# Kernel optimization log

Hardware: AMD Instinct MI355X
Metric: run time of the kernel (lower is better)

Reference implementation:

```python
import jax, jax.numpy as jnp
import numpy as np
import math

B, T, C = 4, 2048, 1024
H = 16
HD = C // H


def setup_inputs() -> dict:
    key = jax.random.key(0)
    k1, k2, k3 = jax.random.split(key, 3)
    sc = 0.02
    return {
        "x": jax.random.normal(k1, (B, T, C), dtype=jnp.float32),
        "w_qkv": jax.random.normal(k2, (3 * C, C), dtype=jnp.float32) * sc,
        "b_qkv": jnp.zeros((3 * C,), dtype=jnp.float32),
        "w_proj": jax.random.normal(k3, (C, C), dtype=jnp.float32) * sc,
        "b_proj": jnp.zeros((C,), dtype=jnp.float32),
    }


def reference(x, w_qkv, b_qkv, w_proj, b_proj):
    b, t, c = x.shape
    qkv = x @ w_qkv.T + b_qkv            # [B,T,3C]
    q, k, v = jnp.split(qkv, 3, axis=2)
    # [B,T,C] -> [B,H,T,HD]
    def heads(z):
        return z.reshape(b, t, H, HD).transpose(0, 2, 1, 3)
    q, k, v = heads(q), heads(k), heads(v)
    att = jnp.einsum('bhqd,bhkd->bhqk', q, k) / math.sqrt(HD)
    causal = jnp.tril(jnp.ones((t, t), dtype=bool))
    att = jnp.where(causal[None, None], att, -jnp.inf)
    att = jax.nn.softmax(att, axis=-1)   # dropout p=0 (eval)
    y = jnp.einsum('bhqk,bhkd->bhqd', att, v)
    y = y.transpose(0, 2, 1, 3).reshape(b, t, c)
    return y @ w_proj.T + b_proj
```

## Files before the change

### kernel.cpp

```cpp
#include <hip/hip_runtime.h>
#include <hip/hip_bf16.h>

#define B_ 4
#define T_ 2048
#define C_ 1024
#define H_ 16
#define HD_ 64
#define M_ (B_*T_)

typedef __attribute__((ext_vector_type(8))) short short8;
typedef __attribute__((ext_vector_type(4))) float f32x4;
typedef __attribute__((ext_vector_type(16))) float f32x16;
typedef __attribute__((ext_vector_type(4))) unsigned int u32x4;
typedef unsigned short u16;
typedef unsigned int u32;

__device__ __forceinline__ u16 f2bf(float f){
  unsigned int x = __builtin_bit_cast(unsigned int, f);
  x += 0x7fffu + ((x >> 16) & 1u);
  return (u16)(x >> 16);
}

__device__ __forceinline__ u32 cvtpk(float lo, float hi){
  u32 r;
  asm("v_cvt_pk_bf16_f32 %0, %1, %2" : "=v"(r) : "v"(lo), "v"(hi));
  return r;
}

#define GLOAD_LDS(gsrc, ldst) \
  __builtin_amdgcn_global_load_lds((const __attribute__((address_space(1))) u32*)(gsrc), \
                                   (__attribute__((address_space(3))) u32*)(ldst), 16, 0, 0)

__global__ __launch_bounds__(256)
void cvt3_kernel(const float* __restrict__ x, const float* __restrict__ w1,
                 const float* __restrict__ w2, u16* __restrict__ xb,
                 u16* __restrict__ w1b, u16* __restrict__ w2b){
  int i = blockIdx.x * 256 + threadIdx.x;
  const float* src; u16* dst; int off;
  if (i < 2097152)              { src = x;  dst = xb;  off = i; }
  else if (i < 2097152 + 786432){ src = w1; dst = w1b; off = i - 2097152; }
  else                          { src = w2; dst = w2b; off = i - (2097152 + 786432); }
  float4 f = reinterpret_cast<const float4*>(src)[off];
  ushort4 u;
  u.x = f2bf(f.x); u.y = f2bf(f.y); u.z = f2bf(f.z); u.w = f2bf(f.w);
  reinterpret_cast<ushort4*>(dst)[off] = u;
}

template<int MODE>
__global__ __launch_bounds__(256)
void gemm_bt(const u16* __restrict__ A, const u16* __restrict__ Bt,
             const float* __restrict__ bias, float* __restrict__ Cf,
             u16* __restrict__ Qo, u16* __restrict__ Ko, u16* __restrict__ Vo,
             int N, int K)
{
  __shared__ u16 As[128 * 64];
  __shared__ u16 Bs[128 * 64];
  const int tid = threadIdx.x;
  const int wave = tid >> 6, lane = tid & 63;
  const int lo = lane & 15, hi = lane >> 4;
  const int wm = (wave >> 1) * 64, wn = (wave & 1) * 64;

  const int nwgx = gridDim.x;
  const int nwg  = gridDim.x * gridDim.y;
  const int flat = blockIdx.y * nwgx + blockIdx.x;
  const int cpx  = nwg >> 3;
  const int swz  = (flat & 7) * cpx + (flat >> 3);
  const long bm = (long)(swz / nwgx) * 128, bn = (long)(swz % nwgx) * 128;

  f32x4 acc[4][4];
  #pragma unroll
  for (int i = 0; i < 4; i++)
    #pragma unroll
    for (int j = 0; j < 4; j++)
      acc[i][j] = (f32x4){0.f, 0.f, 0.f, 0.f};

  for (int k0 = 0; k0 < K; k0 += 64){
    if (k0) __syncthreads();
    #pragma unroll
    for (int j = 0; j < 4; j++){
      int chunk = j * 256 + tid;
      int row = chunk >> 3, cc = (chunk & 7) * 8;
      GLOAD_LDS(&A [(bm + row) * K + k0 + cc], &As[chunk * 8]);
      GLOAD_LDS(&Bt[(bn + row) * K + k0 + cc], &Bs[chunk * 8]);
    }
    __syncthreads();
    #pragma unroll
    for (int kk = 0; kk < 64; kk += 32){
      short8 af[4], bf[4];
      #pragma unroll
      for (int mi = 0; mi < 4; mi++)
        af[mi] = *reinterpret_cast<const short8*>(&As[(wm + mi*16 + lo) * 64 + kk + hi*8]);
      #pragma unroll
      for (int ni = 0; ni < 4; ni++)
        bf[ni] = *reinterpret_cast<const short8*>(&Bs[(wn + ni*16 + lo) * 64 + kk + hi*8]);
      #pragma unroll
      for (int mi = 0; mi < 4; mi++)
        #pragma unroll
        for (int ni = 0; ni < 4; ni++)
          acc[mi][ni] = __builtin_amdgcn_mfma_f32_16x16x32_bf16(af[mi], bf[ni], acc[mi][ni], 0, 0, 0);
    }
  }

  #pragma unroll
  for (int mi = 0; mi < 4; mi++){
    #pragma unroll
    for (int ni = 0; ni < 4; ni++){
      #pragma unroll
      for (int rg = 0; rg < 4; rg++){
        long rowg = bm + wm + mi*16 + hi*4 + rg;
        long colg = bn + wn + ni*16 + lo;
        float v = acc[mi][ni][rg] + bias[colg];
        if (MODE == 0){
          int part = (int)(colg >> 10), cc = (int)(colg & 1023);
          int h = cc >> 6, d = cc & 63;
          long b = rowg >> 11, t = rowg & 2047;
          if (part == 0) v *= 0.18033688f;
          u16* dst = (part == 0) ? Qo : ((part == 1) ? Ko : Vo);
          dst[(((b << 4) + h) * 2048 + t) * 64 + d] = f2bf(v);
        } else {
          Cf[rowg * (long)N + colg] = v;
        }
      }
    }
  }
}

__global__ __launch_bounds__(256)
void vtrans_kernel(const u16* __restrict__ V, u16* __restrict__ Vt){
  __shared__ u16 Ls[64][72];
  const int bh = blockIdx.y;
  const int t0 = blockIdx.x * 64;
  const u16* Vb = V + ((size_t)bh * 2048 + t0) * 64;
  u16* Ob = Vt + (size_t)bh * 64 * 2048 + t0;
  const int r = threadIdx.x >> 3;
  const int c = (threadIdx.x & 7) * 8;
  #pragma unroll
  for (int rr = 0; rr < 64; rr += 32){
    int row = r + rr;
    *reinterpret_cast<short8*>(&Ls[row][c ^ (((row >> 4) & 3) << 4)]) =
      *reinterpret_cast<const short8*>(&Vb[(size_t)row * 64 + c]);
  }
  __syncthreads();
  const int d  = threadIdx.x >> 2;
  const int tc = (threadIdx.x & 3) * 16;
  const int v  = ((tc >> 4) & 3) << 4;
  short8 o0, o1;
  #pragma unroll
  for (int j = 0; j < 8; j++) o0[j] = (short)Ls[tc + j][d ^ v];
  #pragma unroll
  for (int j = 0; j < 8; j++) o1[j] = (short)Ls[tc + 8 + j][d ^ v];
  *reinterpret_cast<short8*>(&Ob[(size_t)d * 2048 + tc]) = o0;
  *reinterpret_cast<short8*>(&Ob[(size_t)d * 2048 + tc + 8]) = o1;
}

__global__ __launch_bounds__(256, 2)
void attn_kernel(const u16* __restrict__ Q, const u16* __restrict__ K,
                 const u16* __restrict__ Vt, u16* __restrict__ Y)
{
  const int blk = blockIdx.x;
  const int bh = (blk & 7) * 8 + ((blk >> 3) & 7);
  const int qg = 15 - (blk >> 6);
  const int tid = threadIdx.x, wave = tid >> 6, lane = tid & 63;
  const int l31 = lane & 31, h5 = lane >> 5;
  const int qc = qg * 4 + wave;
  const int q0w = qc * 32;
  const int qrow = q0w + l31;
  const u16* Qb = Q  + (size_t)bh * 2048 * 64;
  const u16* Kb = K  + (size_t)bh * 2048 * 64;
  const u16* Vb = Vt + (size_t)bh * 64 * 2048;

  short8 qf[4];
  #pragma unroll
  for (int ks = 0; ks < 4; ks++)
    qf[ks] = *reinterpret_cast<const short8*>(&Qb[(size_t)qrow * 64 + ks * 16 + h5 * 8]);

  f32x16 o0, o1;
  #pragma unroll
  for (int i = 0; i < 16; i++){ o0[i] = 0.f; o1[i] = 0.f; }
  float m = -1e30f, l = 0.f;

  const int F = qc >> 1;

  for (int jt = 0; jt <= F; jt++){
    const int k0 = jt << 6;

    short8 kf0[4], kf1[4];
    #pragma unroll
    for (int ks = 0; ks < 4; ks++){
      kf0[ks] = *reinterpret_cast<const short8*>(&Kb[(size_t)(k0 + l31) * 64 + ks * 16 + h5 * 8]);
      kf1[ks] = *reinterpret_cast<const short8*>(&Kb[(size_t)(k0 + 32 + l31) * 64 + ks * 16 + h5 * 8]);
    }
    f32x16 st0, st1;
    #pragma unroll
    for (int i = 0; i < 16; i++){ st0[i] = 0.f; st1[i] = 0.f; }
    __builtin_amdgcn_s_setprio(1);
    #pragma unroll
    for (int ks = 0; ks < 4; ks++)
      st0 = __builtin_amdgcn_mfma_f32_32x32x16_bf16(kf0[ks], qf[ks], st0, 0, 0, 0);
    #pragma unroll
    for (int ks = 0; ks < 4; ks++)
      st1 = __builtin_amdgcn_mfma_f32_32x32x16_bf16(kf1[ks], qf[ks], st1, 0, 0, 0);
    __builtin_amdgcn_s_setprio(0);

    short8 vf0[4], vf1[4];
    #pragma unroll
    for (int ks = 0; ks < 4; ks++){
      vf0[ks] = *reinterpret_cast<const short8*>(&Vb[(size_t)l31 * 2048 + k0 + ks * 16 + h5 * 8]);
      vf1[ks] = *reinterpret_cast<const short8*>(&Vb[(size_t)(32 + l31) * 2048 + k0 + ks * 16 + h5 * 8]);
    }

    if (jt == F){
      #pragma unroll
      for (int r = 0; r < 16; r++){
        int kvr = k0 + (r & 3) + 8 * (r >> 2) + 4 * h5;
        if (kvr > qrow)      st0[r] = -1e30f;
        if (kvr + 32 > qrow) st1[r] = -1e30f;
      }
    }

    float t[16];
    #pragma unroll
    for (int r = 0; r < 16; r++) t[r] = fmaxf(st0[r], st1[r]);
    #pragma unroll
    for (int s = 8; s > 0; s >>= 1)
      #pragma unroll
      for (int r = 0; r < 8; r++) if (r < s) t[r] = fmaxf(t[r], t[r + s]);
    float rm = fmaxf(t[0], __shfl_xor(t[0], 32));
    float mn = fmaxf(m, rm);
    float alpha = __builtin_amdgcn_exp2f(m - mn);
    m = mn;
    float rs = 0.f;
    #pragma unroll
    for (int r = 0; r < 16; r++){
      st0[r] = __builtin_amdgcn_exp2f(st0[r] - mn);
      st1[r] = __builtin_amdgcn_exp2f(st1[r] - mn);
      rs += st0[r] + st1[r];
    }
    rs += __shfl_xor(rs, 32);
    l = l * alpha + rs;
    #pragma unroll
    for (int i = 0; i < 16; i++){ o0[i] *= alpha; o1[i] *= alpha; }

    short8 pa[4];
    #pragma unroll
    for (int ks2 = 0; ks2 < 4; ks2++){
      const f32x16& sv = (ks2 < 2) ? st0 : st1;
      const int gg = 8 * (ks2 & 1);
      u32 w0 = cvtpk(sv[gg + 0], sv[gg + 1]);
      u32 w1 = cvtpk(sv[gg + 2], sv[gg + 3]);
      u32 w2 = cvtpk(sv[gg + 4], sv[gg + 5]);
      u32 w3 = cvtpk(sv[gg + 6], sv[gg + 7]);
      u32 sa = h5 ? w0 : w2;
      u32 sb = h5 ? w1 : w3;
      u32 ra = (u32)__shfl_xor((int)sa, 32);
      u32 rb = (u32)__shfl_xor((int)sb, 32);
      u32x4 pw;
      pw.x = h5 ? ra : w0;
      pw.y = h5 ? rb : w1;
      pw.z = h5 ? w2 : ra;
      pw.w = h5 ? w3 : rb;
      pa[ks2] = __builtin_bit_cast(short8, pw);
    }

    __builtin_amdgcn_s_setprio(1);
    #pragma unroll
    for (int ks = 0; ks < 4; ks++)
      o0 = __builtin_amdgcn_mfma_f32_32x32x16_bf16(vf0[ks], pa[ks], o0, 0, 0, 0);
    #pragma unroll
    for (int ks = 0; ks < 4; ks++)
      o1 = __builtin_amdgcn_mfma_f32_32x32x16_bf16(vf1[ks], pa[ks], o1, 0, 0, 0);
    __builtin_amdgcn_s_setprio(0);
  }

  const int b = bh >> 4, h = bh & 15;
  const float inv = 1.f / l;
  u16* Yr = Y + ((size_t)(b * 2048 + qrow)) * 1024 + h * 64;
  #pragma unroll
  for (int rq = 0; rq < 4; rq++){
    ushort4 ua, ub;
    #pragma unroll
    for (int e = 0; e < 4; e++){
      ((u16*)&ua)[e] = f2bf(o0[rq * 4 + e] * inv);
      ((u16*)&ub)[e] = f2bf(o1[rq * 4 + e] * inv);
    }
    *reinterpret_cast<ushort4*>(&Yr[rq * 8 + h5 * 4])      = ua;
    *reinterpret_cast<ushort4*>(&Yr[32 + rq * 8 + h5 * 4]) = ub;
  }
}

extern "C" void kernel_launch(void* const* d_in, const int* in_sizes, int n_in,
                              void* d_out, int out_size, void* d_ws, size_t ws_size,
                              hipStream_t stream)
{
  const float* x      = (const float*)d_in[0];
  const float* w_qkv  = (const float*)d_in[1];
  const float* b_qkv  = (const float*)d_in[2];
  const float* w_proj = (const float*)d_in[3];
  const float* b_proj = (const float*)d_in[4];
  float* out = (float*)d_out;

  char* ws = (char*)d_ws;
  u16* xb     = (u16*)(ws);
  u16* wqkvb  = (u16*)(ws + (16u << 20));
  u16* wprojb = (u16*)(ws + (22u << 20));
  u16* qb     = (u16*)(ws + (24u << 20));
  u16* kb     = (u16*)(ws + (40u << 20));
  u16* vb     = (u16*)(ws + (56u << 20));
  u16* yb     = (u16*)(ws + (72u << 20));
  u16* vtb    = xb;

  cvt3_kernel<<<12288, 256, 0, stream>>>(x, w_qkv, w_proj, xb, wqkvb, wprojb);

  dim3 g1(3072 / 128, M_ / 128);
  gemm_bt<0><<<g1, 256, 0, stream>>>(xb, wqkvb, b_qkv, nullptr, qb, kb, vb, 3072, C_);

  dim3 gt(T_ / 64, B_ * H_);
  vtrans_kernel<<<gt, 256, 0, stream>>>(vb, vtb);

  attn_kernel<<<1024, 256, 0, stream>>>(qb, kb, vtb, yb);

  dim3 g2(1024 / 128, M_ / 128);
  gemm_bt<1><<<g2, 256, 0, stream>>>(yb, wprojb, b_proj, out, nullptr, nullptr, nullptr, C_, C_);
}
```

Before: 260.1 us.

## Replace GEMM with 256x256 tiled, double-buffered, swizzled-LDS 8-wave kernel

Rewrites both projection GEMMs to use 256x256 output tiles with 512 threads (8 waves, each computing 128x64). Global-to-LDS loads are double-buffered so the next K tile streams in while MFMAs run on the current one, and LDS columns are XOR-swizzled to avoid bank conflicts. Fragment loads are interleaved with MFMA groups under raised wave priority. The aim is higher arithmetic intensity and hidden load latency. The cost is more LDS (128KB) and registers, and far fewer workgroups (128 for the output projection), which risks underfilling the GPU's CUs.

```diff
diff --git a/kernel.cpp b/kernel.cpp
--- a/kernel.cpp
+++ b/kernel.cpp
@@ -47,68 +47,139 @@
 }
 
 template<int MODE>
-__global__ __launch_bounds__(256)
-void gemm_bt(const u16* __restrict__ A, const u16* __restrict__ Bt,
+__global__ __launch_bounds__(512, 2)
+void gemm256(const u16* __restrict__ A, const u16* __restrict__ Bt,
              const float* __restrict__ bias, float* __restrict__ Cf,
              u16* __restrict__ Qo, u16* __restrict__ Ko, u16* __restrict__ Vo,
              int N, int K)
 {
-  __shared__ u16 As[128 * 64];
-  __shared__ u16 Bs[128 * 64];
+  __shared__ u16 As[2 * 16384];
+  __shared__ u16 Bs[2 * 16384];
   const int tid = threadIdx.x;
-  const int wave = tid >> 6, lane = tid & 63;
+  const int wid = tid >> 6, lane = tid & 63;
   const int lo = lane & 15, hi = lane >> 4;
-  const int wm = (wave >> 1) * 64, wn = (wave & 1) * 64;
-
-  const int nwgx = gridDim.x;
-  const int nwg  = gridDim.x * gridDim.y;
-  const int flat = blockIdx.y * nwgx + blockIdx.x;
-  const int cpx  = nwg >> 3;
-  const int swz  = (flat & 7) * cpx + (flat >> 3);
-  const long bm = (long)(swz / nwgx) * 128, bn = (long)(swz % nwgx) * 128;
-
-  f32x4 acc[4][4];
-  #pragma unroll
-  for (int i = 0; i < 4; i++)
-    #pragma unroll
-    for (int j = 0; j < 4; j++)
-      acc[i][j] = (f32x4){0.f, 0.f, 0.f, 0.f};
-
-  for (int k0 = 0; k0 < K; k0 += 64){
-    if (k0) __syncthreads();
-    #pragma unroll
-    for (int j = 0; j < 4; j++){
-      int chunk = j * 256 + tid;
-      int row = chunk >> 3, cc = (chunk & 7) * 8;
-      GLOAD_LDS(&A [(bm + row) * K + k0 + cc], &As[chunk * 8]);
-      GLOAD_LDS(&Bt[(bn + row) * K + k0 + cc], &Bs[chunk * 8]);
-    }
+  const int wr = wid >> 2, wc = wid & 3;
+  const int NBN = N >> 8;
+  const int cpx = gridDim.x >> 3;
+  const int swz = (blockIdx.x & 7) * cpx + (blockIdx.x >> 3);
+  const long bm = (long)(swz / NBN) << 8;
+  const long bn = (long)(swz % NBN) << 8;
+
+  f32x4 acc[8][4];
+  #pragma unroll
+  for (int mi = 0; mi < 8; mi++)
+    #pragma unroll
+    for (int ni = 0; ni < 4; ni++)
+      acc[mi][ni] = (f32x4){0.f, 0.f, 0.f, 0.f};
+
+  #define STAGE256(bufsel, k0s) do {                                           \
+    _Pragma("unroll")                                                          \
+    for (int j = 0; j < 2; j++){                                               \
+      const int row  = j * 64 + (tid >> 3);                                    \
+      const int slot = tid & 7;                                                \
+      const int scol = (slot ^ (row & 7)) << 3;                                \
+      const int doff = (bufsel) * 16384 + ((row << 3) + slot) * 8;             \
+      GLOAD_LDS(&A [(bm +       row) * K + (k0s) + scol], &As[doff]);          \
+      GLOAD_LDS(&A [(bm + 128 + row) * K + (k0s) + scol], &As[doff + 8192]);   \
+      GLOAD_LDS(&Bt[(bn +       row) * K + (k0s) + scol], &Bs[doff]);          \
+      GLOAD_LDS(&Bt[(bn + 128 + row) * K + (k0s) + scol], &Bs[doff + 8192]);   \
+    }                                                                          \
+  } while (0)
+
+  const int NK = K >> 6;
+  STAGE256(0, 0);
+
+  const int sx = lo & 7;
+  short8 af[4][2], bf[2][2];
+
+  for (int kt = 0; kt < NK; kt++){
+    const int cb = kt & 1;
     __syncthreads();
-    #pragma unroll
-    for (int kk = 0; kk < 64; kk += 32){
-      short8 af[4], bf[4];
-      #pragma unroll
-      for (int mi = 0; mi < 4; mi++)
-        af[mi] = *reinterpret_cast<const short8*>(&As[(wm + mi*16 + lo) * 64 + kk + hi*8]);
-      #pragma unroll
-      for (int ni = 0; ni < 4; ni++)
-        bf[ni] = *reinterpret_cast<const short8*>(&Bs[(wn + ni*16 + lo) * 64 + kk + hi*8]);
-      #pragma unroll
-      for (int mi = 0; mi < 4; mi++)
+    if (kt + 1 < NK) STAGE256(cb ^ 1, (kt + 1) << 6);
+
+    const u16* Ab = &As[cb * 16384];
+    const u16* Bb = &Bs[cb * 16384];
+
+    #pragma unroll
+    for (int mi = 0; mi < 4; mi++)
+      #pragma unroll
+      for (int kk = 0; kk < 2; kk++)
+        af[mi][kk] = *reinterpret_cast<const short8*>(
+          &Ab[(wr*128 + mi*16 + lo) * 64 + ((((kk<<2)+hi) ^ sx) << 3)]);
+    #pragma unroll
+    for (int ni = 0; ni < 2; ni++)
+      #pragma unroll
+      for (int kk = 0; kk < 2; kk++)
+        bf[ni][kk] = *reinterpret_cast<const short8*>(
+          &Bb[(wc*64 + ni*16 + lo) * 64 + ((((kk<<2)+hi) ^ sx) << 3)]);
+    __builtin_amdgcn_s_setprio(1);
+    #pragma unroll
+    for (int mi = 0; mi < 4; mi++)
+      #pragma unroll
+      for (int ni = 0; ni < 2; ni++)
         #pragma unroll
-        for (int ni = 0; ni < 4; ni++)
-          acc[mi][ni] = __builtin_amdgcn_mfma_f32_16x16x32_bf16(af[mi], bf[ni], acc[mi][ni], 0, 0, 0);
-    }
-  }
-
-  #pragma unroll
-  for (int mi = 0; mi < 4; mi++){
+        for (int kk = 0; kk < 2; kk++)
+          acc[mi][ni] = __builtin_amdgcn_mfma_f32_16x16x32_bf16(af[mi][kk], bf[ni][kk], acc[mi][ni], 0, 0, 0);
+    __builtin_amdgcn_s_setprio(0);
+
+    #pragma unroll
+    for (int ni = 0; ni < 2; ni++)
+      #pragma unroll
+      for (int kk = 0; kk < 2; kk++)
+        bf[ni][kk] = *reinterpret_cast<const short8*>(
+          &Bb[(wc*64 + (ni+2)*16 + lo) * 64 + ((((kk<<2)+hi) ^ sx) << 3)]);
+    __builtin_amdgcn_s_setprio(1);
+    #pragma unroll
+    for (int mi = 0; mi < 4; mi++)
+      #pragma unroll
+      for (int ni = 0; ni < 2; ni++)
+        #pragma unroll
+        for (int kk = 0; kk < 2; kk++)
+          acc[mi][ni+2] = __builtin_amdgcn_mfma_f32_16x16x32_bf16(af[mi][kk], bf[ni][kk], acc[mi][ni+2], 0, 0, 0);
+    __builtin_amdgcn_s_setprio(0);
+
+    #pragma unroll
+    for (int mi = 0; mi < 4; mi++)
+      #pragma unroll
+      for (int kk = 0; kk < 2; kk++)
+        af[mi][kk] = *reinterpret_cast<const short8*>(
+          &Ab[(wr*128 + (mi+4)*16 + lo) * 64 + ((((kk<<2)+hi) ^ sx) << 3)]);
+    __builtin_amdgcn_s_setprio(1);
+    #pragma unroll
+    for (int mi = 0; mi < 4; mi++)
+      #pragma unroll
+      for (int ni = 0; ni < 2; ni++)
+        #pragma unroll
+        for (int kk = 0; kk < 2; kk++)
+          acc[mi+4][ni+2] = __builtin_amdgcn_mfma_f32_16x16x32_bf16(af[mi][kk], bf[ni][kk], acc[mi+4][ni+2], 0, 0, 0);
+    __builtin_amdgcn_s_setprio(0);
+
+    #pragma unroll
+    for (int ni = 0; ni < 2; ni++)
+      #pragma unroll
+      for (int kk = 0; kk < 2; kk++)
+        bf[ni][kk] = *reinterpret_cast<const short8*>(
+          &Bb[(wc*64 + ni*16 + lo) * 64 + ((((kk<<2)+hi) ^ sx) << 3)]);
+    __builtin_amdgcn_s_setprio(1);
+    #pragma unroll
+    for (int mi = 0; mi < 4; mi++)
+      #pragma unroll
+      for (int ni = 0; ni < 2; ni++)
+        #pragma unroll
+        for (int kk = 0; kk < 2; kk++)
+          acc[mi+4][ni] = __builtin_amdgcn_mfma_f32_16x16x32_bf16(af[mi][kk], bf[ni][kk], acc[mi+4][ni], 0, 0, 0);
+    __builtin_amdgcn_s_setprio(0);
+  }
+  #undef STAGE256
+
+  #pragma unroll
+  for (int mi = 0; mi < 8; mi++){
     #pragma unroll
     for (int ni = 0; ni < 4; ni++){
       #pragma unroll
       for (int rg = 0; rg < 4; rg++){
-        long rowg = bm + wm + mi*16 + hi*4 + rg;
-        long colg = bn + wn + ni*16 + lo;
+        long rowg = bm + wr*128 + mi*16 + hi*4 + rg;
+        long colg = bn + wc*64 + ni*16 + lo;
         float v = acc[mi][ni][rg] + bias[colg];
         if (MODE == 0){
           int part = (int)(colg >> 10), cc = (int)(colg & 1023);
@@ -311,14 +382,12 @@
 
   cvt3_kernel<<<12288, 256, 0, stream>>>(x, w_qkv, w_proj, xb, wqkvb, wprojb);
 
-  dim3 g1(3072 / 128, M_ / 128);
-  gemm_bt<0><<<g1, 256, 0, stream>>>(xb, wqkvb, b_qkv, nullptr, qb, kb, vb, 3072, C_);
+  gemm256<0><<<384, 512, 0, stream>>>(xb, wqkvb, b_qkv, nullptr, qb, kb, vb, 3072, C_);
 
   dim3 gt(T_ / 64, B_ * H_);
   vtrans_kernel<<<gt, 256, 0, stream>>>(vb, vtb);
 
   attn_kernel<<<1024, 256, 0, stream>>>(qb, kb, vtb, yb);
 
-  dim3 g2(1024 / 128, M_ / 128);
-  gemm_bt<1><<<g2, 256, 0, stream>>>(yb, wprojb, b_proj, out, nullptr, nullptr, nullptr, C_, C_);
-}
+  gemm256<1><<<128, 512, 0, stream>>>(yb, wprojb, b_proj, out, nullptr, nullptr, nullptr, C_, C_);
+}
```

Result: no change. 260.1 us (+0.0%).
